# Optimization experiments

Measured on AMD Instinct MI355X. Metric: run time of the kernel, lower is better.

Reference implementation:

```python
import jax, jax.numpy as jnp
import numpy as np

STRIDE = 1
PADDING = 1
DILATION = 1


def setup_inputs() -> dict:
    key = jax.random.key(0)
    k1, k2, k3 = jax.random.split(key, 3)
    b_i, b_j, c, h, w = 32, 1, 128, 32, 32
    oc, kh, kw = 128, 3, 3
    x = jax.random.normal(k1, (b_i, b_j, c, h, w), dtype=jnp.float32)
    weight = jax.random.normal(k2, (b_i, oc, c, kh, kw), dtype=jnp.float32) * 0.05
    bias = jax.random.normal(k3, (b_i, b_j, oc), dtype=jnp.float32) * 0.05
    return {"x": x, "weight": weight, "bias": bias}


def reference(x, weight, bias):
    # x: [b_i, b_j, c, h, w]; weight: [b_i, oc, c, kh, kw]; bias: [b_i, b_j, oc]
    b_i, b_j, c, h, w = x.shape
    oc, kh, kw = weight.shape[1], weight.shape[3], weight.shape[4]
    # fold per-sample dim into channels, run one grouped conv with groups=b_i
    xr = jnp.transpose(x, (1, 0, 2, 3, 4)).reshape(b_j, b_i * c, h, w)
    wr = weight.reshape(b_i * oc, c, kh, kw)
    out = jax.lax.conv_general_dilated(
        xr, wr,
        window_strides=(STRIDE, STRIDE),
        padding=[(PADDING, PADDING), (PADDING, PADDING)],
        rhs_dilation=(DILATION, DILATION),
        dimension_numbers=("NCHW", "OIHW", "NCHW"),
        feature_group_count=b_i,
    )  # [b_j, b_i*oc, H, W]
    H, W = out.shape[-2], out.shape[-1]
    out = out.reshape(b_j, b_i, oc, H, W).transpose(1, 0, 2, 3, 4)  # [b_i, b_j, oc, H, W]
    out = out + bias[:, :, :, None, None]
    return out
```

## Files before the change

kernel.cpp:

```cpp
#include <hip/hip_runtime.h>

typedef unsigned short u16;
typedef unsigned int u32;
typedef __attribute__((ext_vector_type(2))) unsigned int u32x2;
typedef __attribute__((ext_vector_type(8))) short bf16x8;
typedef __attribute__((ext_vector_type(4))) float f32x4;

#define CIN 128
#define OC 128
#define NP 1024
#define KTOT 1152
#define NSTEP 18
#define BK 64
#define TILE_U16 8192
#define SAMP_U16 (NSTEP * TILE_U16)

typedef const u32 __attribute__((address_space(1)))* gptr_t;
typedef u32 __attribute__((address_space(3)))* lptr_t;

__device__ __forceinline__ u16 f2bf(float f) {
  unsigned b = __builtin_bit_cast(unsigned, f);
  b += 0x7fffu + ((b >> 16) & 1u);
  return (u16)(b >> 16);
}

__global__ void wcvt_kernel(const float* __restrict__ w, u16* __restrict__ wbf2) {
  __shared__ u16 lds[KTOT];
  const int blk = blockIdx.x;
  const int t = threadIdx.x;
  const int i = blk >> 7, row = blk & 127;
  const float* src = w + (size_t)blk * KTOT;
#pragma unroll
  for (int e = 0; e < 9; ++e) {
    int idx = t + 128 * e;
    lds[idx] = f2bf(src[idx]);
  }
  __syncthreads();
  u16* dst = wbf2 + (size_t)i * SAMP_U16;
  const int rsw = row & 7;
#pragma unroll
  for (int e = 0; e < 9; ++e) {
    const int o = t + 128 * e;
    const int s = o >> 6;
    const int slotk = (o >> 3) & 7;
    const int ee = o & 7;
    dst[s * TILE_U16 + (row * 8 + (slotk ^ rsw)) * 8 + ee] = lds[t * 9 + e];
  }
}

__global__ __launch_bounds__(128, 1) void conv_mfma(
    const float* __restrict__ x,
    const u16* __restrict__ wbf2,
    const float* __restrict__ bias,
    float* __restrict__ out) {
  __shared__ u16 Xs[4 * 34 * 128];
  __shared__ u16 Asw[2][OC * BK];

  const int wg = (int)blockIdx.x;
  const int swz = (wg & 7) * 64 + (wg >> 3);
  const int i  = swz >> 4;
  const int pt = swz & 15;
  const int p0 = pt * 64;
  const int tid = (int)threadIdx.x;
  const int lane = tid & 63;
  const int wm = tid >> 6;
  const int lcol = lane & 15;
  const int lhi  = lane >> 4;

  const float* xi = x + (size_t)i * CIN * NP;
  const u16*   wt = wbf2 + (size_t)i * SAMP_U16;

#define STAGE(step, buf) do {                                          \
    const char* _tb = (const char*)(wt + (step) * TILE_U16);           \
    _Pragma("unroll")                                                  \
    for (int _j = 0; _j < 8; ++_j) {                                   \
      const int _off = wm * 8192 + _j * 1024;                          \
      __builtin_amdgcn_global_load_lds(                                \
          (gptr_t)(_tb + _off + lane * 16),                            \
          (lptr_t)((char*)&Asw[buf][0] + _off), 16, 0, 0);             \
    }                                                                  \
  } while (0)

  STAGE(0, 0);

  {
    const int xx = tid & 31;
    const int cg = tid >> 5;
    const int col = xx + 1;
    const int csw = col & 7;
#pragma unroll
    for (int r = 0; r < 4; ++r) {
      const int yr = 2 * pt - 1 + r;
      float v[32];
      if ((unsigned)yr < 32u) {
        const float* src = xi + (size_t)(cg * 32) * NP + yr * 32 + xx;
#pragma unroll
        for (int j = 0; j < 32; ++j) v[j] = src[(size_t)j * NP];
      } else {
#pragma unroll
        for (int j = 0; j < 32; ++j) v[j] = 0.f;
      }
      u32 pk[16];
#pragma unroll
      for (int m = 0; m < 16; ++m)
        pk[m] = (u32)f2bf(v[2 * m]) | ((u32)f2bf(v[2 * m + 1]) << 16);
#pragma unroll
      for (int q = 0; q < 8; ++q) {
        const int cslot = cg * 4 + (q >> 1);
        const int idx = ((r * 34 + col) * 16 + (cslot ^ csw)) * 8 + (q & 1) * 4;
        *(u32x2*)(&Xs[idx]) = (u32x2){pk[2 * q], pk[2 * q + 1]};
      }
    }
    {
      const int r = tid >> 5;
      const int hc = ((tid >> 4) & 1) ? 33 : 0;
      const int s = tid & 15;
      const int idx = ((r * 34 + hc) * 16 + (s ^ (hc & 7))) * 8;
      *(bf16x8*)(&Xs[idx]) = (bf16x8){0, 0, 0, 0, 0, 0, 0, 0};
    }
  }

  f32x4 acc[4][4];
#pragma unroll
  for (int mi = 0; mi < 4; ++mi)
#pragma unroll
    for (int ni = 0; ni < 4; ++ni)
      acc[mi][ni] = (f32x4){0.f, 0.f, 0.f, 0.f};

  __syncthreads();

#pragma unroll
  for (int step = 0; step < NSTEP; ++step) {
    const int buf = step & 1;
    const int rs = step >> 1;
    const int r3 = rs / 3;
    const int dy = r3 - 1;
    const int dx = (rs - r3 * 3) - 1;
    const int c0s = (step & 1) * 8;

    if (step + 1 < NSTEP) STAGE(step + 1, buf ^ 1);

    __builtin_amdgcn_s_setprio(1);
#pragma unroll
    for (int kkk = 0; kkk < 2; ++kkk) {
      bf16x8 af[4], bfr[4];
#pragma unroll
      for (int mi = 0; mi < 4; ++mi) {
        const int row = wm * 64 + mi * 16 + lcol;
        const int slot = (kkk * 4 + lhi) ^ (row & 7);
        af[mi] = *(const bf16x8*)(&Asw[buf][row * BK + slot * 8]);
      }
#pragma unroll
      for (int ni = 0; ni < 4; ++ni) {
        const int srow = 1 + (ni >> 1) + dy;
        const int col  = (ni & 1) * 16 + lcol + 1 + dx;
        const int cslot = c0s + kkk * 4 + lhi;
        const int idx = ((srow * 34 + col) * 16 + (cslot ^ (col & 7))) * 8;
        bfr[ni] = *(const bf16x8*)(&Xs[idx]);
      }
#pragma unroll
      for (int mi = 0; mi < 4; ++mi)
#pragma unroll
        for (int ni = 0; ni < 4; ++ni)
          acc[mi][ni] = __builtin_amdgcn_mfma_f32_16x16x32_bf16(
              af[mi], bfr[ni], acc[mi][ni], 0, 0, 0);
    }
    __builtin_amdgcn_s_setprio(0);

    __syncthreads();
  }

  const int row0 = lhi * 4;
#pragma unroll
  for (int mi = 0; mi < 4; ++mi) {
    const int oc = wm * 64 + mi * 16 + row0;
#pragma unroll
    for (int jj = 0; jj < 4; ++jj) {
      const float bv = bias[i * OC + oc + jj];
      float* orow = out + ((size_t)i * OC + oc + jj) * NP;
#pragma unroll
      for (int ni = 0; ni < 4; ++ni) {
        const int pg = p0 + ni * 16 + lcol;
        orow[pg] = acc[mi][ni][jj] + bv;
      }
    }
  }
#undef STAGE
}

extern "C" void kernel_launch(void* const* d_in, const int* in_sizes, int n_in,
                              void* d_out, int out_size, void* d_ws, size_t ws_size,
                              hipStream_t stream) {
  const float* x    = (const float*)d_in[0];
  const float* w    = (const float*)d_in[1];
  const float* bias = (const float*)d_in[2];
  float* out = (float*)d_out;
  u16* wbf2 = (u16*)d_ws;

  wcvt_kernel<<<dim3(32 * OC), dim3(128), 0, stream>>>(w, wbf2);
  conv_mfma<<<dim3(512), dim3(128), 0, stream>>>(x, wbf2, bias, out);
}
```

Measured before the change: 34.90 us.

## Double pixel tile per workgroup, triple-buffer weight staging with vmcnt-based waits

Each workgroup now has four waves covering 128 output pixels, organised as a 2x2 wave grid, instead of two waves covering 64. This halves the grid and halves how often each weight tile is loaded per sample. Weight staging becomes a three-slot ring with two tiles in flight, and the full __syncthreads is replaced by an explicit vmcnt wait plus s_barrier. The cost is fewer workgroups (256 on a large GPU), which lowers occupancy and parallelism, plus more LDS per block.

```diff
diff --git a/kernel.cpp b/kernel.cpp
--- a/kernel.cpp
+++ b/kernel.cpp
@@ -48,22 +48,24 @@
   }
 }
 
-__global__ __launch_bounds__(128, 1) void conv_mfma(
+__global__ __launch_bounds__(256, 1) void conv_mfma(
     const float* __restrict__ x,
     const u16* __restrict__ wbf2,
     const float* __restrict__ bias,
     float* __restrict__ out) {
-  __shared__ u16 Xs[4 * 34 * 128];
-  __shared__ u16 Asw[2][OC * BK];
+  __shared__ u16 Xs[6 * 34 * 128];
+  __shared__ u16 Asw[3][TILE_U16];
 
   const int wg = (int)blockIdx.x;
-  const int swz = (wg & 7) * 64 + (wg >> 3);
-  const int i  = swz >> 4;
-  const int pt = swz & 15;
-  const int p0 = pt * 64;
+  const int swz = (wg & 7) * 32 + (wg >> 3);
+  const int i  = swz >> 3;
+  const int pt = swz & 7;
+  const int p0 = pt * 128;
   const int tid = (int)threadIdx.x;
   const int lane = tid & 63;
-  const int wm = tid >> 6;
+  const int wid = tid >> 6;
+  const int wm = wid >> 1;
+  const int wn = wid & 1;
   const int lcol = lane & 15;
   const int lhi  = lane >> 4;
 
@@ -73,8 +75,8 @@
 #define STAGE(step, buf) do {                                          \
     const char* _tb = (const char*)(wt + (step) * TILE_U16);           \
     _Pragma("unroll")                                                  \
-    for (int _j = 0; _j < 8; ++_j) {                                   \
-      const int _off = wm * 8192 + _j * 1024;                          \
+    for (int _j = 0; _j < 4; ++_j) {                                   \
+      const int _off = wid * 4096 + _j * 1024;                         \
       __builtin_amdgcn_global_load_lds(                                \
           (gptr_t)(_tb + _off + lane * 16),                            \
           (lptr_t)((char*)&Asw[buf][0] + _off), 16, 0, 0);             \
@@ -82,6 +84,7 @@
   } while (0)
 
   STAGE(0, 0);
+  STAGE(1, 1);
 
   {
     const int xx = tid & 31;
@@ -89,30 +92,30 @@
     const int col = xx + 1;
     const int csw = col & 7;
 #pragma unroll
-    for (int r = 0; r < 4; ++r) {
-      const int yr = 2 * pt - 1 + r;
-      float v[32];
+    for (int r = 0; r < 6; ++r) {
+      const int yr = 4 * pt - 1 + r;
+      float v[16];
       if ((unsigned)yr < 32u) {
-        const float* src = xi + (size_t)(cg * 32) * NP + yr * 32 + xx;
-#pragma unroll
-        for (int j = 0; j < 32; ++j) v[j] = src[(size_t)j * NP];
+        const float* src = xi + (size_t)(cg * 16) * NP + yr * 32 + xx;
+#pragma unroll
+        for (int j = 0; j < 16; ++j) v[j] = src[(size_t)j * NP];
       } else {
 #pragma unroll
-        for (int j = 0; j < 32; ++j) v[j] = 0.f;
-      }
-      u32 pk[16];
-#pragma unroll
-      for (int m = 0; m < 16; ++m)
+        for (int j = 0; j < 16; ++j) v[j] = 0.f;
+      }
+      u32 pk[8];
+#pragma unroll
+      for (int m = 0; m < 8; ++m)
         pk[m] = (u32)f2bf(v[2 * m]) | ((u32)f2bf(v[2 * m + 1]) << 16);
 #pragma unroll
-      for (int q = 0; q < 8; ++q) {
-        const int cslot = cg * 4 + (q >> 1);
+      for (int q = 0; q < 4; ++q) {
+        const int cslot = cg * 2 + (q >> 1);
         const int idx = ((r * 34 + col) * 16 + (cslot ^ csw)) * 8 + (q & 1) * 4;
         *(u32x2*)(&Xs[idx]) = (u32x2){pk[2 * q], pk[2 * q + 1]};
       }
     }
-    {
-      const int r = tid >> 5;
+    if (tid < 192) {
+      const int r = tid / 32;
       const int hc = ((tid >> 4) & 1) ? 33 : 0;
       const int s = tid & 15;
       const int idx = ((r * 34 + hc) * 16 + (s ^ (hc & 7))) * 8;
@@ -131,14 +134,14 @@
 
 #pragma unroll
   for (int step = 0; step < NSTEP; ++step) {
-    const int buf = step & 1;
+    const int buf = step % 3;
     const int rs = step >> 1;
     const int r3 = rs / 3;
     const int dy = r3 - 1;
     const int dx = (rs - r3 * 3) - 1;
     const int c0s = (step & 1) * 8;
 
-    if (step + 1 < NSTEP) STAGE(step + 1, buf ^ 1);
+    if (step + 2 < NSTEP) STAGE(step + 2, (step + 2) % 3);
 
     __builtin_amdgcn_s_setprio(1);
 #pragma unroll
@@ -152,7 +155,7 @@
       }
 #pragma unroll
       for (int ni = 0; ni < 4; ++ni) {
-        const int srow = 1 + (ni >> 1) + dy;
+        const int srow = wn * 2 + (ni >> 1) + 1 + dy;
         const int col  = (ni & 1) * 16 + lcol + 1 + dx;
         const int cslot = c0s + kkk * 4 + lhi;
         const int idx = ((srow * 34 + col) * 16 + (cslot ^ (col & 7))) * 8;
@@ -167,7 +170,15 @@
     }
     __builtin_amdgcn_s_setprio(0);
 
-    __syncthreads();
+    if (step + 2 < NSTEP) {
+      asm volatile("s_waitcnt vmcnt(4)" ::: "memory");
+    } else if (step + 1 < NSTEP) {
+      asm volatile("s_waitcnt vmcnt(0)" ::: "memory");
+    }
+    if (step + 1 < NSTEP) {
+      __builtin_amdgcn_s_barrier();
+      __builtin_amdgcn_sched_barrier(0);
+    }
   }
 
   const int row0 = lhi * 4;
@@ -180,7 +191,7 @@
       float* orow = out + ((size_t)i * OC + oc + jj) * NP;
 #pragma unroll
       for (int ni = 0; ni < 4; ++ni) {
-        const int pg = p0 + ni * 16 + lcol;
+        const int pg = p0 + wn * 64 + ni * 16 + lcol;
         orow[pg] = acc[mi][ni][jj] + bv;
       }
     }
@@ -198,5 +209,5 @@
   u16* wbf2 = (u16*)d_ws;
 
   wcvt_kernel<<<dim3(32 * OC), dim3(128), 0, stream>>>(w, wbf2);
-  conv_mfma<<<dim3(512), dim3(128), 0, stream>>>(x, wbf2, bias, out);
-}
+  conv_mfma<<<dim3(256), dim3(256), 0, stream>>>(x, wbf2, bias, out);
+}
```

After: 33.90 us. 2.9% less time.
